# Optimization experiments

Measured on AMD Instinct MI355X. Metric: run time of the kernel, lower is better.

## Reference

```python
import jax, jax.numpy as jnp
import numpy as np

B, N, S, K, D = 8, 8192, 1024, 32, 64
RADIUS = 0.2
MLP = [64, 64, 128]
C_IN = 3 + D


def _fps(pts):
    # pts: [N,3] -> [S] farthest-point indices (deterministic start at index 0,
    # matching pytorch3d.sample_farthest_points default random_start_point=False)
    def body(carry, _):
        d, last = carry
        dd = jnp.sum((pts - pts[last]) ** 2, axis=-1)
        d = jnp.minimum(d, dd)
        return (d, jnp.argmax(d)), last
    init = (jnp.full((pts.shape[0],), 1e10, pts.dtype), jnp.asarray(0))
    _, idxs = jax.lax.scan(body, init, None, length=S)
    return idxs


def _ball_query(new_xyz, xyz):
    # new_xyz [B,S,3], xyz [B,N,3] -> idx [B,S,K]
    # classic PointNet++ ball query: first K points (by index order) within radius;
    # queries with fewer than K neighbors are padded by replicating the first hit.
    sqr = jnp.sum((new_xyz[:, :, None, :] - xyz[:, None, :, :]) ** 2, axis=-1)  # [B,S,N]
    cand = jnp.where(sqr <= RADIUS ** 2,
                     jnp.arange(N, dtype=jnp.int32)[None, None, :],
                     jnp.int32(N))
    idx = -jax.lax.top_k(-cand, K)[0]  # K smallest valid indices, ascending
    first = idx[..., :1]
    return jnp.where(idx == N, first, idx)


def _gather(arr, idx):
    # arr [B,N,C], idx [B,S,K] -> [B,S,K,C]
    return jax.vmap(lambda a, i: a[i])(arr, idx)


def _forward(xyz, points, attention, w0, b0, w1, b1, w2, b2):
    x = xyz.transpose(0, 2, 1)        # [B,N,3]
    p = points.transpose(0, 2, 1)     # [B,N,D]
    a = attention.transpose(0, 2, 1)  # [B,N,1]
    fps_idx = jax.vmap(_fps)(x)                      # [B,S]
    new_xyz = jax.vmap(lambda q, i: q[i])(x, fps_idx)  # [B,S,3]
    idx = _ball_query(new_xyz, x)                    # [B,S,K]
    g_norm = _gather(x, idx) - new_xyz[:, :, None, :]   # [B,S,K,3]
    feat = jnp.concatenate([g_norm, _gather(p, idx)], axis=-1)  # [B,S,K,3+D]
    new_att = jnp.mean(_gather(a, idx), axis=-2).reshape(x.shape[0], 1, -1)  # [B,1,S]
    # shared MLP (1x1 Conv2d == per-point dense), no BN (bn=False)
    h = jax.nn.relu(jnp.einsum('bskc,oc->bsko', feat, w0) + b0)
    h = jax.nn.relu(jnp.einsum('bskc,oc->bsko', h, w1) + b1)
    h = jax.nn.relu(jnp.einsum('bskc,oc->bsko', h, w2) + b2)
    new_points = jnp.max(h, axis=2)  # max-pool over nsample -> [B,S,C_out]
    return new_xyz.transpose(0, 2, 1), new_points.transpose(0, 2, 1), new_att


def setup_inputs() -> dict:
    key = jax.random.key(0)
    ks = jax.random.split(key, 9)
    xyz = jax.random.uniform(ks[0], (B, 3, N), dtype=jnp.float32)  # unit cube
    points = jax.random.normal(ks[1], (B, D, N), dtype=jnp.float32)
    attention = jax.random.uniform(ks[2], (B, 1, N), dtype=jnp.float32)
    cin = C_IN
    w0 = jax.random.normal(ks[3], (MLP[0], cin), dtype=jnp.float32) / np.sqrt(cin)
    b0 = jnp.zeros((MLP[0],), jnp.float32)
    w1 = jax.random.normal(ks[4], (MLP[1], MLP[0]), dtype=jnp.float32) / np.sqrt(MLP[0])
    b1 = jnp.zeros((MLP[1],), jnp.float32)
    w2 = jax.random.normal(ks[5], (MLP[2], MLP[1]), dtype=jnp.float32) / np.sqrt(MLP[1])
    b2 = jnp.zeros((MLP[2],), jnp.float32)
    return {"xyz": xyz, "points": points, "attention": attention,
            "w0": w0, "b0": b0, "w1": w1, "b1": b1, "w2": w2, "b2": b2}


def reference(xyz, points, attention, w0, b0, w1, b1, w2, b2):
    return _forward(xyz, points, attention, w0, b0, w1, b1, w2, b2)
```

## Files before the change

kernel.cpp:

```cpp
#include <hip/hip_runtime.h>

#define NPTS 8192
#define NSAMP 1024
#define NBATCH 8
#define KNB 32

typedef float f32x2 __attribute__((ext_vector_type(2)));
typedef unsigned long long u64;

__device__ __forceinline__ f32x2 pk_add(f32x2 a, f32x2 b) {
  f32x2 d; asm("v_pk_add_f32 %0, %1, %2" : "=v"(d) : "v"(a), "v"(b)); return d;
}
__device__ __forceinline__ f32x2 pk_mul(f32x2 a, f32x2 b) {
  f32x2 d; asm("v_pk_mul_f32 %0, %1, %2" : "=v"(d) : "v"(a), "v"(b)); return d;
}

#define DPP_FMAX_ROUND(v, CTRL)                                                        \
  do {                                                                                 \
    int _b = __float_as_int(v);                                                        \
    int _p = __builtin_amdgcn_update_dpp(_b, _b, CTRL, 0xF, 0xF, false);               \
    (v) = fmaxf((v), __int_as_float(_p));                                              \
  } while (0)

#define DPP_FMIN_ROUND(v, CTRL)                                                        \
  do {                                                                                 \
    int _b = __float_as_int(v);                                                        \
    int _p = __builtin_amdgcn_update_dpp(_b, _b, CTRL, 0xF, 0xF, false);               \
    (v) = fminf((v), __int_as_float(_p));                                              \
  } while (0)

#define DPP_UMIN_ROUND(v, CTRL)                                                        \
  do {                                                                                 \
    unsigned _p = (unsigned)__builtin_amdgcn_update_dpp((int)(v), (int)(v), CTRL,      \
                                                        0xF, 0xF, false);              \
    if (_p < (v)) (v) = _p;                                                            \
  } while (0)

#define DPP_MIN_ROUND(k, CTRL)                                                         \
  do {                                                                                 \
    unsigned _lo = (unsigned)(k), _hi = (unsigned)((k) >> 32);                         \
    unsigned _plo = (unsigned)__builtin_amdgcn_update_dpp((int)_lo, (int)_lo, CTRL,    \
                                                          0xF, 0xF, false);            \
    unsigned _phi = (unsigned)__builtin_amdgcn_update_dpp((int)_hi, (int)_hi, CTRL,    \
                                                          0xF, 0xF, false);            \
    u64 _ok = (((u64)_phi) << 32) | _plo;                                              \
    if (_ok < (k)) (k) = _ok;                                                          \
  } while (0)

__device__ __forceinline__ float sqdist_rn(float px, float py, float pz,
                                           float qx, float qy, float qz) {
  float dx = px - qx, dy = py - qy, dz = pz - qz;
  return __fadd_rn(__fadd_rn(__fmul_rn(dx, dx), __fmul_rn(dy, dy)), __fmul_rn(dz, dz));
}

__global__ __launch_bounds__(512) void fps_kernel(const float* __restrict__ xyz,
                                                  float* __restrict__ out_newxyz) {
  __shared__ __align__(16) char smem_raw[NPTS * 3 * 4];
  u64* sbuf = reinterpret_cast<u64*>(smem_raw);
  float* cds = reinterpret_cast<float*>(smem_raw);
  __shared__ u64 wkeys[2][8];

  const int b = blockIdx.x;
  const int tid = threadIdx.x;
  const int lane = tid & 63;
  const int wv = tid >> 6;
  const float* xb = xyz + (size_t)b * 3 * NPTS;

  for (int j = 0; j < 16; j++) {
    int n = tid + j * 512;
    float x = xb[n];
    sbuf[n] = (((u64)__float_as_uint(x)) << 32) | (u64)n;
  }
  __syncthreads();

  for (unsigned k = 2; k <= (unsigned)NPTS; k <<= 1) {
    for (unsigned jm = k >> 1; jm > 0; jm >>= 1) {
      for (int p = 0; p < 16; p++) {
        unsigned i = (unsigned)tid + (unsigned)p * 512u;
        unsigned ixj = i ^ jm;
        if (ixj > i) {
          u64 a = sbuf[i], c = sbuf[ixj];
          bool up = ((i & k) == 0);
          if ((a > c) == up) { sbuf[i] = c; sbuf[ixj] = a; }
        }
      }
      __syncthreads();
    }
  }

  f32x2 X2[8], Y2[8], Z2[8], D2[8];
  unsigned idxp[8];
  float txmin = 1e30f, txmax = -1e30f;
#pragma unroll
  for (int j = 0; j < 8; j++) {
    u64 k0 = sbuf[tid * 16 + 2 * j];
    u64 k1 = sbuf[tid * 16 + 2 * j + 1];
    unsigned n0 = (unsigned)k0 & 8191u, n1 = (unsigned)k1 & 8191u;
    float x0 = __uint_as_float((unsigned)(k0 >> 32));
    float x1 = __uint_as_float((unsigned)(k1 >> 32));
    X2[j].x = x0; X2[j].y = x1;
    Y2[j].x = xb[NPTS + n0];     Y2[j].y = xb[NPTS + n1];
    Z2[j].x = xb[2 * NPTS + n0]; Z2[j].y = xb[2 * NPTS + n1];
    D2[j].x = 1e10f;             D2[j].y = 1e10f;
    idxp[j] = n0 | (n1 << 16);
    txmin = fminf(txmin, fminf(x0, x1));
    txmax = fmaxf(txmax, fmaxf(x0, x1));
  }
  DPP_FMIN_ROUND(txmin, 0x111); DPP_FMIN_ROUND(txmin, 0x112);
  DPP_FMIN_ROUND(txmin, 0x114); DPP_FMIN_ROUND(txmin, 0x118);
  DPP_FMIN_ROUND(txmin, 0x142); DPP_FMIN_ROUND(txmin, 0x143);
  DPP_FMAX_ROUND(txmax, 0x111); DPP_FMAX_ROUND(txmax, 0x112);
  DPP_FMAX_ROUND(txmax, 0x114); DPP_FMAX_ROUND(txmax, 0x118);
  DPP_FMAX_ROUND(txmax, 0x142); DPP_FMAX_ROUND(txmax, 0x143);
  const float xlo = __int_as_float(__builtin_amdgcn_readlane(__float_as_int(txmin), 63));
  const float xhi = __int_as_float(__builtin_amdgcn_readlane(__float_as_int(txmax), 63));
  __syncthreads();

#pragma unroll
  for (int j = 0; j < 8; j++) {
    unsigned n0 = idxp[j] & 0xFFFFu, n1 = idxp[j] >> 16;
    cds[n0 * 3 + 0] = X2[j].x; cds[n0 * 3 + 1] = Y2[j].x; cds[n0 * 3 + 2] = Z2[j].x;
    cds[n1 * 3 + 0] = X2[j].y; cds[n1 * 3 + 1] = Y2[j].y; cds[n1 * 3 + 2] = Z2[j].y;
  }
  __syncthreads();

  float sx = cds[0], sy = cds[1], sz = cds[2];
  unsigned c0i = 0, c1i = 0;
  float bv_cache = 1e10f;
  u64 key_cache = ~0ull;

  for (int t = 0; t < NSAMP; t++) {
    float gap = fmaxf(fmaxf(xlo - sx, sx - xhi), 0.0f);
    float lb = __fmul_rn(gap, gap);

    if (lb < bv_cache) {
      f32x2 nqx, nqy, nqz;
      nqx.x = -sx; nqx.y = -sx;
      nqy.x = -sy; nqy.y = -sy;
      nqz.x = -sz; nqz.y = -sz;
      float bvx = -1.0f, bvy = -1.0f;
#pragma unroll
      for (int j = 0; j < 8; j++) {
        f32x2 dx = pk_add(X2[j], nqx);
        f32x2 dy = pk_add(Y2[j], nqy);
        f32x2 dz = pk_add(Z2[j], nqz);
        f32x2 dd = pk_add(pk_add(pk_mul(dx, dx), pk_mul(dy, dy)), pk_mul(dz, dz));
        float m0 = fminf(D2[j].x, dd.x);
        float m1 = fminf(D2[j].y, dd.y);
        D2[j].x = m0;
        D2[j].y = m1;
        bvx = fmaxf(bvx, m0);
        bvy = fmaxf(bvy, m1);
      }
      float bv = fmaxf(bvx, bvy);

      DPP_FMAX_ROUND(bv, 0x111);
      DPP_FMAX_ROUND(bv, 0x112);
      DPP_FMAX_ROUND(bv, 0x114);
      DPP_FMAX_ROUND(bv, 0x118);
      DPP_FMAX_ROUND(bv, 0x142);
      DPP_FMAX_ROUND(bv, 0x143);
      float wval = __int_as_float(__builtin_amdgcn_readlane(__float_as_int(bv), 63));

      unsigned cand = 0xFFFFFFFFu;
#pragma unroll
      for (int j = 0; j < 8; j++) {
        unsigned n0 = idxp[j] & 0xFFFFu, n1 = idxp[j] >> 16;
        if (D2[j].x == wval && n0 < cand) cand = n0;
        if (D2[j].y == wval && n1 < cand) cand = n1;
      }
      DPP_UMIN_ROUND(cand, 0x111);
      DPP_UMIN_ROUND(cand, 0x112);
      DPP_UMIN_ROUND(cand, 0x114);
      DPP_UMIN_ROUND(cand, 0x118);
      DPP_UMIN_ROUND(cand, 0x142);
      DPP_UMIN_ROUND(cand, 0x143);

      key_cache = (((u64)(~__float_as_uint(wval))) << 32) | (u64)cand;
      bv_cache = wval;
    }

    const int par = t & 1;
    if (lane == 63) wkeys[par][wv] = key_cache;
    __syncthreads();
    u64 k8 = wkeys[par][lane & 7];
    DPP_MIN_ROUND(k8, 0xB1);
    DPP_MIN_ROUND(k8, 0x4E);
    DPP_MIN_ROUND(k8, 0x141);
    unsigned wid = (unsigned)__builtin_amdgcn_readfirstlane((int)(unsigned)k8);

    if (t + 1 == tid) c0i = wid;
    if (t + 1 == tid + 512) c1i = wid;

    sx = cds[wid * 3 + 0];
    sy = cds[wid * 3 + 1];
    sz = cds[wid * 3 + 2];
  }

  {
    float ax = cds[c0i * 3 + 0], ay = cds[c0i * 3 + 1], az = cds[c0i * 3 + 2];
    float bx = cds[c1i * 3 + 0], by = cds[c1i * 3 + 1], bz = cds[c1i * 3 + 2];
    out_newxyz[(b * 3 + 0) * NSAMP + tid] = ax;
    out_newxyz[(b * 3 + 1) * NSAMP + tid] = ay;
    out_newxyz[(b * 3 + 2) * NSAMP + tid] = az;
    out_newxyz[(b * 3 + 0) * NSAMP + 512 + tid] = bx;
    out_newxyz[(b * 3 + 1) * NSAMP + 512 + tid] = by;
    out_newxyz[(b * 3 + 2) * NSAMP + 512 + tid] = bz;
  }
}

__global__ __launch_bounds__(256) void ballq_kernel(const float* __restrict__ xyz,
                                                    const float* __restrict__ att,
                                                    const float* __restrict__ newxyz,
                                                    int* __restrict__ idx_out,
                                                    float* __restrict__ att_out) {
  __shared__ int rowbuf[4][KNB];
  const int wv = threadIdx.x >> 6;
  const int lane = threadIdx.x & 63;
  const int g = blockIdx.x * 4 + wv;
  const int b = g >> 10;
  const int s = g & 1023;
  const float* xb = xyz + (size_t)b * 3 * NPTS;

  float qx = newxyz[(b * 3 + 0) * NSAMP + s];
  float qy = newxyz[(b * 3 + 1) * NSAMP + s];
  float qz = newxyz[(b * 3 + 2) * NSAMP + s];

  int have = 0;
  int firstn = 0;
  for (int c = 0; c < NPTS / 64; c++) {
    int n = c * 64 + lane;
    float dd = sqdist_rn(xb[n], xb[NPTS + n], xb[2 * NPTS + n], qx, qy, qz);
    bool inb = (dd <= 0.04f);
    unsigned long long m = __ballot(inb);
    if (have == 0 && m != 0ull) firstn = c * 64 + __builtin_ctzll(m);
    int pre = __popcll(m & ((1ull << lane) - 1ull));
    if (inb && (have + pre) < KNB) rowbuf[wv][have + pre] = n;
    have += __popcll(m);
    if (have >= KNB) break;
  }
  if (have > KNB) have = KNB;
  if (lane < KNB && lane >= have) rowbuf[wv][lane] = firstn;

  float av = 0.0f;
  if (lane < KNB) {
    int myidx = rowbuf[wv][lane];
    idx_out[(size_t)g * KNB + lane] = myidx;
    av = att[(size_t)b * NPTS + myidx];
  }
#pragma unroll
  for (int m = 1; m < 64; m <<= 1) av += __shfl_xor(av, m, 64);
  if (lane == 0) att_out[g] = av * 0.03125f;
}

__global__ __launch_bounds__(256) void mlp_kernel(
    const float* __restrict__ xyz, const float* __restrict__ pts,
    const float* __restrict__ newxyz, const int* __restrict__ idx,
    const float* __restrict__ w0, const float* __restrict__ b0,
    const float* __restrict__ w1, const float* __restrict__ b1,
    const float* __restrict__ w2, const float* __restrict__ b2,
    float* __restrict__ out_np) {
  const int g = blockIdx.x;
  const int b = g >> 10;
  const int s = g & 1023;
  const int t = threadIdx.x;

  __shared__ __align__(16) float feat[67 * 32];
  __shared__ __align__(16) float h0s[64 * 36];
  __shared__ __align__(16) float h1s[64 * 36];
  __shared__ int sidx[KNB];

  if (t < KNB) sidx[t] = idx[(size_t)g * KNB + t];
  __syncthreads();

  {
    int k = t & 31, rg = t >> 5;
    int n = sidx[k];
    const float* pb = pts + (size_t)b * 64 * NPTS;
    for (int r = rg; r < 67; r += 8) {
      float v;
      if (r < 3)
        v = xyz[((size_t)b * 3 + r) * NPTS + n] - newxyz[(b * 3 + r) * NSAMP + s];
      else
        v = pb[(size_t)(r - 3) * NPTS + n];
      feat[r * 32 + k] = v;
    }
  }
  __syncthreads();

  const int kq = t & 7;
  const int og = t >> 3;

  {
    float a0[8];
    float bu = b0[2 * og], bw = b0[2 * og + 1];
    a0[0] = a0[1] = a0[2] = a0[3] = bu;
    a0[4] = a0[5] = a0[6] = a0[7] = bw;
    const float* wr0 = w0 + (2 * og) * 67;
    const float* wr1 = wr0 + 67;
    for (int c = 0; c < 67; c++) {
      float4 f = *(const float4*)&feat[c * 32 + kq * 4];
      float u = wr0[c], v = wr1[c];
      a0[0] = fmaf(u, f.x, a0[0]); a0[1] = fmaf(u, f.y, a0[1]);
      a0[2] = fmaf(u, f.z, a0[2]); a0[3] = fmaf(u, f.w, a0[3]);
      a0[4] = fmaf(v, f.x, a0[4]); a0[5] = fmaf(v, f.y, a0[5]);
      a0[6] = fmaf(v, f.z, a0[6]); a0[7] = fmaf(v, f.w, a0[7]);
    }
    float4 r0, r1;
    r0.x = fmaxf(a0[0], 0.f); r0.y = fmaxf(a0[1], 0.f);
    r0.z = fmaxf(a0[2], 0.f); r0.w = fmaxf(a0[3], 0.f);
    r1.x = fmaxf(a0[4], 0.f); r1.y = fmaxf(a0[5], 0.f);
    r1.z = fmaxf(a0[6], 0.f); r1.w = fmaxf(a0[7], 0.f);
    *(float4*)&h0s[(2 * og) * 36 + kq * 4] = r0;
    *(float4*)&h0s[(2 * og + 1) * 36 + kq * 4] = r1;
  }
  __syncthreads();

  {
    float a1[8];
    float bu = b1[2 * og], bw = b1[2 * og + 1];
    a1[0] = a1[1] = a1[2] = a1[3] = bu;
    a1[4] = a1[5] = a1[6] = a1[7] = bw;
    const float* wr0 = w1 + (2 * og) * 64;
    const float* wr1 = wr0 + 64;
    for (int c = 0; c < 64; c++) {
      float4 f = *(const float4*)&h0s[c * 36 + kq * 4];
      float u = wr0[c], v = wr1[c];
      a1[0] = fmaf(u, f.x, a1[0]); a1[1] = fmaf(u, f.y, a1[1]);
      a1[2] = fmaf(u, f.z, a1[2]); a1[3] = fmaf(u, f.w, a1[3]);
      a1[4] = fmaf(v, f.x, a1[4]); a1[5] = fmaf(v, f.y, a1[5]);
      a1[6] = fmaf(v, f.z, a1[6]); a1[7] = fmaf(v, f.w, a1[7]);
    }
    float4 r0, r1;
    r0.x = fmaxf(a1[0], 0.f); r0.y = fmaxf(a1[1], 0.f);
    r0.z = fmaxf(a1[2], 0.f); r0.w = fmaxf(a1[3], 0.f);
    r1.x = fmaxf(a1[4], 0.f); r1.y = fmaxf(a1[5], 0.f);
    r1.z = fmaxf(a1[6], 0.f); r1.w = fmaxf(a1[7], 0.f);
    *(float4*)&h1s[(2 * og) * 36 + kq * 4] = r0;
    *(float4*)&h1s[(2 * og + 1) * 36 + kq * 4] = r1;
  }
  __syncthreads();

  {
    const int kq2 = t & 3;
    const int og2 = t >> 2;
    float a2[16];
    float bu = b2[2 * og2], bw = b2[2 * og2 + 1];
#pragma unroll
    for (int i = 0; i < 8; i++) { a2[i] = bu; a2[8 + i] = bw; }
    const float* wr0 = w2 + (2 * og2) * 64;
    const float* wr1 = wr0 + 64;
    for (int c = 0; c < 64; c++) {
      float4 fA = *(const float4*)&h1s[c * 36 + kq2 * 8];
      float4 fB = *(const float4*)&h1s[c * 36 + kq2 * 8 + 4];
      float u = wr0[c], v = wr1[c];
      a2[0] = fmaf(u, fA.x, a2[0]);  a2[1] = fmaf(u, fA.y, a2[1]);
      a2[2] = fmaf(u, fA.z, a2[2]);  a2[3] = fmaf(u, fA.w, a2[3]);
      a2[4] = fmaf(u, fB.x, a2[4]);  a2[5] = fmaf(u, fB.y, a2[5]);
      a2[6] = fmaf(u, fB.z, a2[6]);  a2[7] = fmaf(u, fB.w, a2[7]);
      a2[8] = fmaf(v, fA.x, a2[8]);  a2[9] = fmaf(v, fA.y, a2[9]);
      a2[10] = fmaf(v, fA.z, a2[10]); a2[11] = fmaf(v, fA.w, a2[11]);
      a2[12] = fmaf(v, fB.x, a2[12]); a2[13] = fmaf(v, fB.y, a2[13]);
      a2[14] = fmaf(v, fB.z, a2[14]); a2[15] = fmaf(v, fB.w, a2[15]);
    }
    float m0 = a2[0], m1 = a2[8];
#pragma unroll
    for (int i = 1; i < 8; i++) { m0 = fmaxf(m0, a2[i]); m1 = fmaxf(m1, a2[8 + i]); }
    m0 = fmaxf(m0, 0.f);
    m1 = fmaxf(m1, 0.f);
    m0 = fmaxf(m0, __shfl_xor(m0, 1, 64));
    m0 = fmaxf(m0, __shfl_xor(m0, 2, 64));
    m1 = fmaxf(m1, __shfl_xor(m1, 1, 64));
    m1 = fmaxf(m1, __shfl_xor(m1, 2, 64));
    if (kq2 == 0) {
      out_np[((size_t)b * 128 + 2 * og2) * NSAMP + s] = m0;
      out_np[((size_t)b * 128 + 2 * og2 + 1) * NSAMP + s] = m1;
    }
  }
}

extern "C" void kernel_launch(void* const* d_in, const int* in_sizes, int n_in,
                              void* d_out, int out_size, void* d_ws, size_t ws_size,
                              hipStream_t stream) {
  (void)in_sizes; (void)n_in; (void)out_size; (void)ws_size;
  const float* xyz = (const float*)d_in[0];
  const float* pts = (const float*)d_in[1];
  const float* att = (const float*)d_in[2];
  const float* w0 = (const float*)d_in[3];
  const float* b0 = (const float*)d_in[4];
  const float* w1 = (const float*)d_in[5];
  const float* b1 = (const float*)d_in[6];
  const float* w2 = (const float*)d_in[7];
  const float* b2 = (const float*)d_in[8];

  float* out = (float*)d_out;
  float* out_newxyz = out;
  float* out_newpts = out + NBATCH * 3 * NSAMP;
  float* out_att = out + NBATCH * 3 * NSAMP + NBATCH * 128 * NSAMP;
  int* idx_ws = (int*)d_ws;

  fps_kernel<<<NBATCH, 512, 0, stream>>>(xyz, out_newxyz);
  ballq_kernel<<<(NBATCH * NSAMP) / 4, 256, 0, stream>>>(xyz, att, out_newxyz, idx_ws, out_att);
  mlp_kernel<<<NBATCH * NSAMP, 256, 0, stream>>>(xyz, pts, out_newxyz, idx_ws,
                                                 w0, b0, w1, b1, w2, b2, out_newpts);
}
```

Measured before the change: 1.160 ms.

## Fuse FPS, ball query and MLP into persistent producer-consumer kernel

Merges the three kernels into one persistent launch. 8 blocks run farthest-point sampling and publish progress per batch through atomics in global memory. 120 consumer blocks poll that progress and run ball query plus the MLP on pairs of samples as soon as they are available. This overlaps the serial FPS stage with downstream work and removes the index workspace round trip. The cost is fewer consumer blocks, spin-wait overhead, and a deadlock risk if producer and consumer blocks are not co-resident.

```diff
diff --git a/kernel.cpp b/kernel.cpp
--- a/kernel.cpp
+++ b/kernel.cpp
@@ -4,6 +4,8 @@
 #define NSAMP 1024
 #define NBATCH 8
 #define KNB 32
+#define NPROD 8
+#define NCONS 120
 
 typedef float f32x2 __attribute__((ext_vector_type(2)));
 typedef unsigned long long u64;
@@ -53,328 +55,324 @@
   return __fadd_rn(__fadd_rn(__fmul_rn(dx, dx), __fmul_rn(dy, dy)), __fmul_rn(dz, dz));
 }
 
-__global__ __launch_bounds__(512) void fps_kernel(const float* __restrict__ xyz,
-                                                  float* __restrict__ out_newxyz) {
-  __shared__ __align__(16) char smem_raw[NPTS * 3 * 4];
-  u64* sbuf = reinterpret_cast<u64*>(smem_raw);
-  float* cds = reinterpret_cast<float*>(smem_raw);
-  __shared__ u64 wkeys[2][8];
-
-  const int b = blockIdx.x;
-  const int tid = threadIdx.x;
-  const int lane = tid & 63;
-  const int wv = tid >> 6;
-  const float* xb = xyz + (size_t)b * 3 * NPTS;
-
-  for (int j = 0; j < 16; j++) {
-    int n = tid + j * 512;
-    float x = xb[n];
-    sbuf[n] = (((u64)__float_as_uint(x)) << 32) | (u64)n;
-  }
-  __syncthreads();
-
-  for (unsigned k = 2; k <= (unsigned)NPTS; k <<= 1) {
-    for (unsigned jm = k >> 1; jm > 0; jm >>= 1) {
-      for (int p = 0; p < 16; p++) {
-        unsigned i = (unsigned)tid + (unsigned)p * 512u;
-        unsigned ixj = i ^ jm;
-        if (ixj > i) {
-          u64 a = sbuf[i], c = sbuf[ixj];
-          bool up = ((i & k) == 0);
-          if ((a > c) == up) { sbuf[i] = c; sbuf[ixj] = a; }
-        }
-      }
-      __syncthreads();
-    }
-  }
-
-  f32x2 X2[8], Y2[8], Z2[8], D2[8];
-  unsigned idxp[8];
-  float txmin = 1e30f, txmax = -1e30f;
-#pragma unroll
-  for (int j = 0; j < 8; j++) {
-    u64 k0 = sbuf[tid * 16 + 2 * j];
-    u64 k1 = sbuf[tid * 16 + 2 * j + 1];
-    unsigned n0 = (unsigned)k0 & 8191u, n1 = (unsigned)k1 & 8191u;
-    float x0 = __uint_as_float((unsigned)(k0 >> 32));
-    float x1 = __uint_as_float((unsigned)(k1 >> 32));
-    X2[j].x = x0; X2[j].y = x1;
-    Y2[j].x = xb[NPTS + n0];     Y2[j].y = xb[NPTS + n1];
-    Z2[j].x = xb[2 * NPTS + n0]; Z2[j].y = xb[2 * NPTS + n1];
-    D2[j].x = 1e10f;             D2[j].y = 1e10f;
-    idxp[j] = n0 | (n1 << 16);
-    txmin = fminf(txmin, fminf(x0, x1));
-    txmax = fmaxf(txmax, fmaxf(x0, x1));
-  }
-  DPP_FMIN_ROUND(txmin, 0x111); DPP_FMIN_ROUND(txmin, 0x112);
-  DPP_FMIN_ROUND(txmin, 0x114); DPP_FMIN_ROUND(txmin, 0x118);
-  DPP_FMIN_ROUND(txmin, 0x142); DPP_FMIN_ROUND(txmin, 0x143);
-  DPP_FMAX_ROUND(txmax, 0x111); DPP_FMAX_ROUND(txmax, 0x112);
-  DPP_FMAX_ROUND(txmax, 0x114); DPP_FMAX_ROUND(txmax, 0x118);
-  DPP_FMAX_ROUND(txmax, 0x142); DPP_FMAX_ROUND(txmax, 0x143);
-  const float xlo = __int_as_float(__builtin_amdgcn_readlane(__float_as_int(txmin), 63));
-  const float xhi = __int_as_float(__builtin_amdgcn_readlane(__float_as_int(txmax), 63));
-  __syncthreads();
-
-#pragma unroll
-  for (int j = 0; j < 8; j++) {
-    unsigned n0 = idxp[j] & 0xFFFFu, n1 = idxp[j] >> 16;
-    cds[n0 * 3 + 0] = X2[j].x; cds[n0 * 3 + 1] = Y2[j].x; cds[n0 * 3 + 2] = Z2[j].x;
-    cds[n1 * 3 + 0] = X2[j].y; cds[n1 * 3 + 1] = Y2[j].y; cds[n1 * 3 + 2] = Z2[j].y;
-  }
-  __syncthreads();
-
-  float sx = cds[0], sy = cds[1], sz = cds[2];
-  unsigned c0i = 0, c1i = 0;
-  float bv_cache = 1e10f;
-  u64 key_cache = ~0ull;
-
-  for (int t = 0; t < NSAMP; t++) {
-    float gap = fmaxf(fmaxf(xlo - sx, sx - xhi), 0.0f);
-    float lb = __fmul_rn(gap, gap);
-
-    if (lb < bv_cache) {
-      f32x2 nqx, nqy, nqz;
-      nqx.x = -sx; nqx.y = -sx;
-      nqy.x = -sy; nqy.y = -sy;
-      nqz.x = -sz; nqz.y = -sz;
-      float bvx = -1.0f, bvy = -1.0f;
-#pragma unroll
-      for (int j = 0; j < 8; j++) {
-        f32x2 dx = pk_add(X2[j], nqx);
-        f32x2 dy = pk_add(Y2[j], nqy);
-        f32x2 dz = pk_add(Z2[j], nqz);
-        f32x2 dd = pk_add(pk_add(pk_mul(dx, dx), pk_mul(dy, dy)), pk_mul(dz, dz));
-        float m0 = fminf(D2[j].x, dd.x);
-        float m1 = fminf(D2[j].y, dd.y);
-        D2[j].x = m0;
-        D2[j].y = m1;
-        bvx = fmaxf(bvx, m0);
-        bvy = fmaxf(bvy, m1);
-      }
-      float bv = fmaxf(bvx, bvy);
-
-      DPP_FMAX_ROUND(bv, 0x111);
-      DPP_FMAX_ROUND(bv, 0x112);
-      DPP_FMAX_ROUND(bv, 0x114);
-      DPP_FMAX_ROUND(bv, 0x118);
-      DPP_FMAX_ROUND(bv, 0x142);
-      DPP_FMAX_ROUND(bv, 0x143);
-      float wval = __int_as_float(__builtin_amdgcn_readlane(__float_as_int(bv), 63));
-
-      unsigned cand = 0xFFFFFFFFu;
-#pragma unroll
-      for (int j = 0; j < 8; j++) {
-        unsigned n0 = idxp[j] & 0xFFFFu, n1 = idxp[j] >> 16;
-        if (D2[j].x == wval && n0 < cand) cand = n0;
-        if (D2[j].y == wval && n1 < cand) cand = n1;
-      }
-      DPP_UMIN_ROUND(cand, 0x111);
-      DPP_UMIN_ROUND(cand, 0x112);
-      DPP_UMIN_ROUND(cand, 0x114);
-      DPP_UMIN_ROUND(cand, 0x118);
-      DPP_UMIN_ROUND(cand, 0x142);
-      DPP_UMIN_ROUND(cand, 0x143);
-
-      key_cache = (((u64)(~__float_as_uint(wval))) << 32) | (u64)cand;
-      bv_cache = wval;
-    }
-
-    const int par = t & 1;
-    if (lane == 63) wkeys[par][wv] = key_cache;
-    __syncthreads();
-    u64 k8 = wkeys[par][lane & 7];
-    DPP_MIN_ROUND(k8, 0xB1);
-    DPP_MIN_ROUND(k8, 0x4E);
-    DPP_MIN_ROUND(k8, 0x141);
-    unsigned wid = (unsigned)__builtin_amdgcn_readfirstlane((int)(unsigned)k8);
-
-    if (t + 1 == tid) c0i = wid;
-    if (t + 1 == tid + 512) c1i = wid;
-
-    sx = cds[wid * 3 + 0];
-    sy = cds[wid * 3 + 1];
-    sz = cds[wid * 3 + 2];
-  }
-
-  {
-    float ax = cds[c0i * 3 + 0], ay = cds[c0i * 3 + 1], az = cds[c0i * 3 + 2];
-    float bx = cds[c1i * 3 + 0], by = cds[c1i * 3 + 1], bz = cds[c1i * 3 + 2];
-    out_newxyz[(b * 3 + 0) * NSAMP + tid] = ax;
-    out_newxyz[(b * 3 + 1) * NSAMP + tid] = ay;
-    out_newxyz[(b * 3 + 2) * NSAMP + tid] = az;
-    out_newxyz[(b * 3 + 0) * NSAMP + 512 + tid] = bx;
-    out_newxyz[(b * 3 + 1) * NSAMP + 512 + tid] = by;
-    out_newxyz[(b * 3 + 2) * NSAMP + 512 + tid] = bz;
-  }
-}
-
-__global__ __launch_bounds__(256) void ballq_kernel(const float* __restrict__ xyz,
-                                                    const float* __restrict__ att,
-                                                    const float* __restrict__ newxyz,
-                                                    int* __restrict__ idx_out,
-                                                    float* __restrict__ att_out) {
-  __shared__ int rowbuf[4][KNB];
-  const int wv = threadIdx.x >> 6;
-  const int lane = threadIdx.x & 63;
-  const int g = blockIdx.x * 4 + wv;
-  const int b = g >> 10;
-  const int s = g & 1023;
-  const float* xb = xyz + (size_t)b * 3 * NPTS;
-
-  float qx = newxyz[(b * 3 + 0) * NSAMP + s];
-  float qy = newxyz[(b * 3 + 1) * NSAMP + s];
-  float qz = newxyz[(b * 3 + 2) * NSAMP + s];
-
-  int have = 0;
-  int firstn = 0;
-  for (int c = 0; c < NPTS / 64; c++) {
-    int n = c * 64 + lane;
-    float dd = sqdist_rn(xb[n], xb[NPTS + n], xb[2 * NPTS + n], qx, qy, qz);
-    bool inb = (dd <= 0.04f);
-    unsigned long long m = __ballot(inb);
-    if (have == 0 && m != 0ull) firstn = c * 64 + __builtin_ctzll(m);
-    int pre = __popcll(m & ((1ull << lane) - 1ull));
-    if (inb && (have + pre) < KNB) rowbuf[wv][have + pre] = n;
-    have += __popcll(m);
-    if (have >= KNB) break;
-  }
-  if (have > KNB) have = KNB;
-  if (lane < KNB && lane >= have) rowbuf[wv][lane] = firstn;
-
-  float av = 0.0f;
-  if (lane < KNB) {
-    int myidx = rowbuf[wv][lane];
-    idx_out[(size_t)g * KNB + lane] = myidx;
-    av = att[(size_t)b * NPTS + myidx];
-  }
-#pragma unroll
-  for (int m = 1; m < 64; m <<= 1) av += __shfl_xor(av, m, 64);
-  if (lane == 0) att_out[g] = av * 0.03125f;
-}
-
-__global__ __launch_bounds__(256) void mlp_kernel(
+__global__ __launch_bounds__(512, 1) void fused_kernel(
     const float* __restrict__ xyz, const float* __restrict__ pts,
-    const float* __restrict__ newxyz, const int* __restrict__ idx,
+    const float* __restrict__ att,
     const float* __restrict__ w0, const float* __restrict__ b0,
     const float* __restrict__ w1, const float* __restrict__ b1,
     const float* __restrict__ w2, const float* __restrict__ b2,
-    float* __restrict__ out_np) {
-  const int g = blockIdx.x;
-  const int b = g >> 10;
-  const int s = g & 1023;
-  const int t = threadIdx.x;
-
-  __shared__ __align__(16) float feat[67 * 32];
-  __shared__ __align__(16) float h0s[64 * 36];
-  __shared__ __align__(16) float h1s[64 * 36];
-  __shared__ int sidx[KNB];
-
-  if (t < KNB) sidx[t] = idx[(size_t)g * KNB + t];
-  __syncthreads();
-
-  {
-    int k = t & 31, rg = t >> 5;
-    int n = sidx[k];
-    const float* pb = pts + (size_t)b * 64 * NPTS;
-    for (int r = rg; r < 67; r += 8) {
-      float v;
-      if (r < 3)
-        v = xyz[((size_t)b * 3 + r) * NPTS + n] - newxyz[(b * 3 + r) * NSAMP + s];
-      else
-        v = pb[(size_t)(r - 3) * NPTS + n];
-      feat[r * 32 + k] = v;
-    }
-  }
-  __syncthreads();
-
-  const int kq = t & 7;
-  const int og = t >> 3;
-
-  {
-    float a0[8];
-    float bu = b0[2 * og], bw = b0[2 * og + 1];
-    a0[0] = a0[1] = a0[2] = a0[3] = bu;
-    a0[4] = a0[5] = a0[6] = a0[7] = bw;
-    const float* wr0 = w0 + (2 * og) * 67;
-    const float* wr1 = wr0 + 67;
-    for (int c = 0; c < 67; c++) {
-      float4 f = *(const float4*)&feat[c * 32 + kq * 4];
-      float u = wr0[c], v = wr1[c];
-      a0[0] = fmaf(u, f.x, a0[0]); a0[1] = fmaf(u, f.y, a0[1]);
-      a0[2] = fmaf(u, f.z, a0[2]); a0[3] = fmaf(u, f.w, a0[3]);
-      a0[4] = fmaf(v, f.x, a0[4]); a0[5] = fmaf(v, f.y, a0[5]);
-      a0[6] = fmaf(v, f.z, a0[6]); a0[7] = fmaf(v, f.w, a0[7]);
-    }
-    float4 r0, r1;
-    r0.x = fmaxf(a0[0], 0.f); r0.y = fmaxf(a0[1], 0.f);
-    r0.z = fmaxf(a0[2], 0.f); r0.w = fmaxf(a0[3], 0.f);
-    r1.x = fmaxf(a0[4], 0.f); r1.y = fmaxf(a0[5], 0.f);
-    r1.z = fmaxf(a0[6], 0.f); r1.w = fmaxf(a0[7], 0.f);
-    *(float4*)&h0s[(2 * og) * 36 + kq * 4] = r0;
-    *(float4*)&h0s[(2 * og + 1) * 36 + kq * 4] = r1;
-  }
-  __syncthreads();
-
-  {
-    float a1[8];
-    float bu = b1[2 * og], bw = b1[2 * og + 1];
-    a1[0] = a1[1] = a1[2] = a1[3] = bu;
-    a1[4] = a1[5] = a1[6] = a1[7] = bw;
-    const float* wr0 = w1 + (2 * og) * 64;
-    const float* wr1 = wr0 + 64;
-    for (int c = 0; c < 64; c++) {
-      float4 f = *(const float4*)&h0s[c * 36 + kq * 4];
-      float u = wr0[c], v = wr1[c];
-      a1[0] = fmaf(u, f.x, a1[0]); a1[1] = fmaf(u, f.y, a1[1]);
-      a1[2] = fmaf(u, f.z, a1[2]); a1[3] = fmaf(u, f.w, a1[3]);
-      a1[4] = fmaf(v, f.x, a1[4]); a1[5] = fmaf(v, f.y, a1[5]);
-      a1[6] = fmaf(v, f.z, a1[6]); a1[7] = fmaf(v, f.w, a1[7]);
-    }
-    float4 r0, r1;
-    r0.x = fmaxf(a1[0], 0.f); r0.y = fmaxf(a1[1], 0.f);
-    r0.z = fmaxf(a1[2], 0.f); r0.w = fmaxf(a1[3], 0.f);
-    r1.x = fmaxf(a1[4], 0.f); r1.y = fmaxf(a1[5], 0.f);
-    r1.z = fmaxf(a1[6], 0.f); r1.w = fmaxf(a1[7], 0.f);
-    *(float4*)&h1s[(2 * og) * 36 + kq * 4] = r0;
-    *(float4*)&h1s[(2 * og + 1) * 36 + kq * 4] = r1;
-  }
-  __syncthreads();
-
-  {
-    const int kq2 = t & 3;
-    const int og2 = t >> 2;
-    float a2[16];
-    float bu = b2[2 * og2], bw = b2[2 * og2 + 1];
-#pragma unroll
-    for (int i = 0; i < 8; i++) { a2[i] = bu; a2[8 + i] = bw; }
-    const float* wr0 = w2 + (2 * og2) * 64;
-    const float* wr1 = wr0 + 64;
-    for (int c = 0; c < 64; c++) {
-      float4 fA = *(const float4*)&h1s[c * 36 + kq2 * 8];
-      float4 fB = *(const float4*)&h1s[c * 36 + kq2 * 8 + 4];
-      float u = wr0[c], v = wr1[c];
-      a2[0] = fmaf(u, fA.x, a2[0]);  a2[1] = fmaf(u, fA.y, a2[1]);
-      a2[2] = fmaf(u, fA.z, a2[2]);  a2[3] = fmaf(u, fA.w, a2[3]);
-      a2[4] = fmaf(u, fB.x, a2[4]);  a2[5] = fmaf(u, fB.y, a2[5]);
-      a2[6] = fmaf(u, fB.z, a2[6]);  a2[7] = fmaf(u, fB.w, a2[7]);
-      a2[8] = fmaf(v, fA.x, a2[8]);  a2[9] = fmaf(v, fA.y, a2[9]);
-      a2[10] = fmaf(v, fA.z, a2[10]); a2[11] = fmaf(v, fA.w, a2[11]);
-      a2[12] = fmaf(v, fB.x, a2[12]); a2[13] = fmaf(v, fB.y, a2[13]);
-      a2[14] = fmaf(v, fB.z, a2[14]); a2[15] = fmaf(v, fB.w, a2[15]);
-    }
-    float m0 = a2[0], m1 = a2[8];
-#pragma unroll
-    for (int i = 1; i < 8; i++) { m0 = fmaxf(m0, a2[i]); m1 = fmaxf(m1, a2[8 + i]); }
-    m0 = fmaxf(m0, 0.f);
-    m1 = fmaxf(m1, 0.f);
-    m0 = fmaxf(m0, __shfl_xor(m0, 1, 64));
-    m0 = fmaxf(m0, __shfl_xor(m0, 2, 64));
-    m1 = fmaxf(m1, __shfl_xor(m1, 1, 64));
-    m1 = fmaxf(m1, __shfl_xor(m1, 2, 64));
-    if (kq2 == 0) {
-      out_np[((size_t)b * 128 + 2 * og2) * NSAMP + s] = m0;
-      out_np[((size_t)b * 128 + 2 * og2 + 1) * NSAMP + s] = m1;
+    float* __restrict__ out_newxyz, float* __restrict__ out_np,
+    float* __restrict__ att_out, unsigned* __restrict__ prog) {
+  __shared__ __align__(16) char smem_raw[98304];
+  __shared__ u64 wkeys[2][8];
+  __shared__ int sidxs[2][KNB];
+
+  const int tid = threadIdx.x;
+
+  if (blockIdx.x < NPROD) {
+    u64* sbuf = reinterpret_cast<u64*>(smem_raw);
+    float* cds = reinterpret_cast<float*>(smem_raw);
+
+    const int b = blockIdx.x;
+    const int lane = tid & 63;
+    const int wv = tid >> 6;
+    const float* xb = xyz + (size_t)b * 3 * NPTS;
+
+    for (int j = 0; j < 16; j++) {
+      int n = tid + j * 512;
+      float x = xb[n];
+      sbuf[n] = (((u64)__float_as_uint(x)) << 32) | (u64)n;
+    }
+    __syncthreads();
+
+    for (unsigned k = 2; k <= (unsigned)NPTS; k <<= 1) {
+      for (unsigned jm = k >> 1; jm > 0; jm >>= 1) {
+        for (int p = 0; p < 16; p++) {
+          unsigned i = (unsigned)tid + (unsigned)p * 512u;
+          unsigned ixj = i ^ jm;
+          if (ixj > i) {
+            u64 a = sbuf[i], c = sbuf[ixj];
+            bool up = ((i & k) == 0);
+            if ((a > c) == up) { sbuf[i] = c; sbuf[ixj] = a; }
+          }
+        }
+        __syncthreads();
+      }
+    }
+
+    f32x2 X2[8], Y2[8], Z2[8], D2[8];
+    unsigned idxp[8];
+    float txmin = 1e30f, txmax = -1e30f;
+#pragma unroll
+    for (int j = 0; j < 8; j++) {
+      u64 k0 = sbuf[tid * 16 + 2 * j];
+      u64 k1 = sbuf[tid * 16 + 2 * j + 1];
+      unsigned n0 = (unsigned)k0 & 8191u, n1 = (unsigned)k1 & 8191u;
+      float x0 = __uint_as_float((unsigned)(k0 >> 32));
+      float x1 = __uint_as_float((unsigned)(k1 >> 32));
+      X2[j].x = x0; X2[j].y = x1;
+      Y2[j].x = xb[NPTS + n0];     Y2[j].y = xb[NPTS + n1];
+      Z2[j].x = xb[2 * NPTS + n0]; Z2[j].y = xb[2 * NPTS + n1];
+      D2[j].x = 1e10f;             D2[j].y = 1e10f;
+      idxp[j] = n0 | (n1 << 16);
+      txmin = fminf(txmin, fminf(x0, x1));
+      txmax = fmaxf(txmax, fmaxf(x0, x1));
+    }
+    DPP_FMIN_ROUND(txmin, 0x111); DPP_FMIN_ROUND(txmin, 0x112);
+    DPP_FMIN_ROUND(txmin, 0x114); DPP_FMIN_ROUND(txmin, 0x118);
+    DPP_FMIN_ROUND(txmin, 0x142); DPP_FMIN_ROUND(txmin, 0x143);
+    DPP_FMAX_ROUND(txmax, 0x111); DPP_FMAX_ROUND(txmax, 0x112);
+    DPP_FMAX_ROUND(txmax, 0x114); DPP_FMAX_ROUND(txmax, 0x118);
+    DPP_FMAX_ROUND(txmax, 0x142); DPP_FMAX_ROUND(txmax, 0x143);
+    const float xlo = __int_as_float(__builtin_amdgcn_readlane(__float_as_int(txmin), 63));
+    const float xhi = __int_as_float(__builtin_amdgcn_readlane(__float_as_int(txmax), 63));
+    __syncthreads();
+
+#pragma unroll
+    for (int j = 0; j < 8; j++) {
+      unsigned n0 = idxp[j] & 0xFFFFu, n1 = idxp[j] >> 16;
+      cds[n0 * 3 + 0] = X2[j].x; cds[n0 * 3 + 1] = Y2[j].x; cds[n0 * 3 + 2] = Z2[j].x;
+      cds[n1 * 3 + 0] = X2[j].y; cds[n1 * 3 + 1] = Y2[j].y; cds[n1 * 3 + 2] = Z2[j].y;
+    }
+    __syncthreads();
+
+    float sx = cds[0], sy = cds[1], sz = cds[2];
+    float bv_cache = 1e10f;
+    u64 key_cache = ~0ull;
+
+    for (int t = 0; t < NSAMP; t++) {
+      if (tid == 0) {
+        out_newxyz[(b * 3 + 0) * NSAMP + t] = sx;
+        out_newxyz[(b * 3 + 1) * NSAMP + t] = sy;
+        out_newxyz[(b * 3 + 2) * NSAMP + t] = sz;
+      }
+
+      float gap = fmaxf(fmaxf(xlo - sx, sx - xhi), 0.0f);
+      float lb = __fmul_rn(gap, gap);
+
+      if (lb < bv_cache) {
+        f32x2 nqx, nqy, nqz;
+        nqx.x = -sx; nqx.y = -sx;
+        nqy.x = -sy; nqy.y = -sy;
+        nqz.x = -sz; nqz.y = -sz;
+        float bvx = -1.0f, bvy = -1.0f;
+#pragma unroll
+        for (int j = 0; j < 8; j++) {
+          f32x2 dx = pk_add(X2[j], nqx);
+          f32x2 dy = pk_add(Y2[j], nqy);
+          f32x2 dz = pk_add(Z2[j], nqz);
+          f32x2 dd = pk_add(pk_add(pk_mul(dx, dx), pk_mul(dy, dy)), pk_mul(dz, dz));
+          float m0 = fminf(D2[j].x, dd.x);
+          float m1 = fminf(D2[j].y, dd.y);
+          D2[j].x = m0;
+          D2[j].y = m1;
+          bvx = fmaxf(bvx, m0);
+          bvy = fmaxf(bvy, m1);
+        }
+        float bv = fmaxf(bvx, bvy);
+
+        DPP_FMAX_ROUND(bv, 0x111);
+        DPP_FMAX_ROUND(bv, 0x112);
+        DPP_FMAX_ROUND(bv, 0x114);
+        DPP_FMAX_ROUND(bv, 0x118);
+        DPP_FMAX_ROUND(bv, 0x142);
+        DPP_FMAX_ROUND(bv, 0x143);
+        float wval = __int_as_float(__builtin_amdgcn_readlane(__float_as_int(bv), 63));
+
+        unsigned cand = 0xFFFFFFFFu;
+#pragma unroll
+        for (int j = 0; j < 8; j++) {
+          unsigned n0 = idxp[j] & 0xFFFFu, n1 = idxp[j] >> 16;
+          if (D2[j].y == wval && n1 < cand) cand = n1;
+          if (D2[j].x == wval && n0 < cand) cand = n0;
+        }
+        DPP_UMIN_ROUND(cand, 0x111);
+        DPP_UMIN_ROUND(cand, 0x112);
+        DPP_UMIN_ROUND(cand, 0x114);
+        DPP_UMIN_ROUND(cand, 0x118);
+        DPP_UMIN_ROUND(cand, 0x142);
+        DPP_UMIN_ROUND(cand, 0x143);
+
+        key_cache = (((u64)(~__float_as_uint(wval))) << 32) | (u64)cand;
+        bv_cache = wval;
+        if (lane == 63) wkeys[t & 1][wv] = key_cache;
+      } else {
+        if (lane == 63) wkeys[t & 1][wv] = key_cache;
+      }
+      __syncthreads();
+      u64 k8 = wkeys[t & 1][lane & 7];
+      DPP_MIN_ROUND(k8, 0xB1);
+      DPP_MIN_ROUND(k8, 0x4E);
+      DPP_MIN_ROUND(k8, 0x141);
+      unsigned wid = (unsigned)__builtin_amdgcn_readfirstlane((int)(unsigned)k8);
+
+      sx = cds[wid * 3 + 0];
+      sy = cds[wid * 3 + 1];
+      sz = cds[wid * 3 + 2];
+
+      if ((t & 7) == 7 && tid == 0) {
+        __threadfence();
+        atomicExch(&prog[b], (unsigned)(t + 1));
+      }
+    }
+  } else {
+    float* smemF = reinterpret_cast<float*>(smem_raw);
+    const int tm = tid >> 8;
+    const int t = tid & 255;
+    float* feat = smemF + tm * 6784;
+    float* h0s = feat + 2144;
+    float* h1s = h0s + 2304;
+
+    for (int p = (int)blockIdx.x - NPROD; p < (NBATCH * NSAMP) / 2; p += NCONS) {
+      const int gA = 2 * p;
+      const int b = gA >> 10;
+      const int sA = gA & 1023;
+      if (tid == 0) {
+        unsigned need = (unsigned)(sA + 2);
+        while (atomicAdd(&prog[b], 0u) < need) __builtin_amdgcn_s_sleep(64);
+        __threadfence();
+      }
+      __syncthreads();
+
+      const int g = gA + tm;
+      const int s = sA + tm;
+      const float* xb = xyz + (size_t)b * 3 * NPTS;
+
+      if (t < 64) {
+        const int lane = t;
+        float qx = out_newxyz[(b * 3 + 0) * NSAMP + s];
+        float qy = out_newxyz[(b * 3 + 1) * NSAMP + s];
+        float qz = out_newxyz[(b * 3 + 2) * NSAMP + s];
+        int have = 0;
+        int firstn = 0;
+        for (int c = 0; c < NPTS / 64; c++) {
+          int n = c * 64 + lane;
+          float dd = sqdist_rn(xb[n], xb[NPTS + n], xb[2 * NPTS + n], qx, qy, qz);
+          bool inb = (dd <= 0.04f);
+          unsigned long long m = __ballot(inb);
+          if (have == 0 && m != 0ull) firstn = c * 64 + __builtin_ctzll(m);
+          int pre = __popcll(m & ((1ull << lane) - 1ull));
+          if (inb && (have + pre) < KNB) sidxs[tm][have + pre] = n;
+          have += __popcll(m);
+          if (have >= KNB) break;
+        }
+        if (have > KNB) have = KNB;
+        if (lane < KNB && lane >= have) sidxs[tm][lane] = firstn;
+
+        float av = 0.0f;
+        if (lane < KNB) av = att[(size_t)b * NPTS + sidxs[tm][lane]];
+#pragma unroll
+        for (int m = 1; m < 64; m <<= 1) av += __shfl_xor(av, m, 64);
+        if (lane == 0) att_out[g] = av * 0.03125f;
+      }
+      __syncthreads();
+
+      {
+        int k = t & 31, rg = t >> 5;
+        int n = sidxs[tm][k];
+        const float* pb = pts + (size_t)b * 64 * NPTS;
+        for (int r = rg; r < 67; r += 8) {
+          float v;
+          if (r < 3)
+            v = xyz[((size_t)b * 3 + r) * NPTS + n] -
+                out_newxyz[(b * 3 + r) * NSAMP + s];
+          else
+            v = pb[(size_t)(r - 3) * NPTS + n];
+          feat[r * 32 + k] = v;
+        }
+      }
+      __syncthreads();
+
+      const int kq = t & 7;
+      const int og = t >> 3;
+
+      {
+        float a0[8];
+        float bu = b0[2 * og], bw = b0[2 * og + 1];
+        a0[0] = a0[1] = a0[2] = a0[3] = bu;
+        a0[4] = a0[5] = a0[6] = a0[7] = bw;
+        const float* wr0 = w0 + (2 * og) * 67;
+        const float* wr1 = wr0 + 67;
+        for (int c = 0; c < 67; c++) {
+          float4 f = *(const float4*)&feat[c * 32 + kq * 4];
+          float u = wr0[c], v = wr1[c];
+          a0[0] = fmaf(u, f.x, a0[0]); a0[1] = fmaf(u, f.y, a0[1]);
+          a0[2] = fmaf(u, f.z, a0[2]); a0[3] = fmaf(u, f.w, a0[3]);
+          a0[4] = fmaf(v, f.x, a0[4]); a0[5] = fmaf(v, f.y, a0[5]);
+          a0[6] = fmaf(v, f.z, a0[6]); a0[7] = fmaf(v, f.w, a0[7]);
+        }
+        float4 r0, r1;
+        r0.x = fmaxf(a0[0], 0.f); r0.y = fmaxf(a0[1], 0.f);
+        r0.z = fmaxf(a0[2], 0.f); r0.w = fmaxf(a0[3], 0.f);
+        r1.x = fmaxf(a0[4], 0.f); r1.y = fmaxf(a0[5], 0.f);
+        r1.z = fmaxf(a0[6], 0.f); r1.w = fmaxf(a0[7], 0.f);
+        *(float4*)&h0s[(2 * og) * 36 + kq * 4] = r0;
+        *(float4*)&h0s[(2 * og + 1) * 36 + kq * 4] = r1;
+      }
+      __syncthreads();
+
+      {
+        float a1[8];
+        float bu = b1[2 * og], bw = b1[2 * og + 1];
+        a1[0] = a1[1] = a1[2] = a1[3] = bu;
+        a1[4] = a1[5] = a1[6] = a1[7] = bw;
+        const float* wr0 = w1 + (2 * og) * 64;
+        const float* wr1 = wr0 + 64;
+        for (int c = 0; c < 64; c++) {
+          float4 f = *(const float4*)&h0s[c * 36 + kq * 4];
+          float u = wr0[c], v = wr1[c];
+          a1[0] = fmaf(u, f.x, a1[0]); a1[1] = fmaf(u, f.y, a1[1]);
+          a1[2] = fmaf(u, f.z, a1[2]); a1[3] = fmaf(u, f.w, a1[3]);
+          a1[4] = fmaf(v, f.x, a1[4]); a1[5] = fmaf(v, f.y, a1[5]);
+          a1[6] = fmaf(v, f.z, a1[6]); a1[7] = fmaf(v, f.w, a1[7]);
+        }
+        float4 r0, r1;
+        r0.x = fmaxf(a1[0], 0.f); r0.y = fmaxf(a1[1], 0.f);
+        r0.z = fmaxf(a1[2], 0.f); r0.w = fmaxf(a1[3], 0.f);
+        r1.x = fmaxf(a1[4], 0.f); r1.y = fmaxf(a1[5], 0.f);
+        r1.z = fmaxf(a1[6], 0.f); r1.w = fmaxf(a1[7], 0.f);
+        *(float4*)&h1s[(2 * og) * 36 + kq * 4] = r0;
+        *(float4*)&h1s[(2 * og + 1) * 36 + kq * 4] = r1;
+      }
+      __syncthreads();
+
+      {
+        const int kq2 = t & 3;
+        const int og2 = t >> 2;
+        float a2[16];
+        float bu = b2[2 * og2], bw = b2[2 * og2 + 1];
+#pragma unroll
+        for (int i = 0; i < 8; i++) { a2[i] = bu; a2[8 + i] = bw; }
+        const float* wr0 = w2 + (2 * og2) * 64;
+        const float* wr1 = wr0 + 64;
+        for (int c = 0; c < 64; c++) {
+          float4 fA = *(const float4*)&h1s[c * 36 + kq2 * 8];
+          float4 fB = *(const float4*)&h1s[c * 36 + kq2 * 8 + 4];
+          float u = wr0[c], v = wr1[c];
+          a2[0] = fmaf(u, fA.x, a2[0]);  a2[1] = fmaf(u, fA.y, a2[1]);
+          a2[2] = fmaf(u, fA.z, a2[2]);  a2[3] = fmaf(u, fA.w, a2[3]);
+          a2[4] = fmaf(u, fB.x, a2[4]);  a2[5] = fmaf(u, fB.y, a2[5]);
+          a2[6] = fmaf(u, fB.z, a2[6]);  a2[7] = fmaf(u, fB.w, a2[7]);
+          a2[8] = fmaf(v, fA.x, a2[8]);  a2[9] = fmaf(v, fA.y, a2[9]);
+          a2[10] = fmaf(v, fA.z, a2[10]); a2[11] = fmaf(v, fA.w, a2[11]);
+          a2[12] = fmaf(v, fB.x, a2[12]); a2[13] = fmaf(v, fB.y, a2[13]);
+          a2[14] = fmaf(v, fB.z, a2[14]); a2[15] = fmaf(v, fB.w, a2[15]);
+        }
+        float m0 = a2[0], m1 = a2[8];
+#pragma unroll
+        for (int i = 1; i < 8; i++) { m0 = fmaxf(m0, a2[i]); m1 = fmaxf(m1, a2[8 + i]); }
+        m0 = fmaxf(m0, 0.f);
+        m1 = fmaxf(m1, 0.f);
+        m0 = fmaxf(m0, __shfl_xor(m0, 1, 64));
+        m0 = fmaxf(m0, __shfl_xor(m0, 2, 64));
+        m1 = fmaxf(m1, __shfl_xor(m1, 1, 64));
+        m1 = fmaxf(m1, __shfl_xor(m1, 2, 64));
+        if (kq2 == 0) {
+          out_np[((size_t)b * 128 + 2 * og2) * NSAMP + s] = m0;
+          out_np[((size_t)b * 128 + 2 * og2 + 1) * NSAMP + s] = m1;
+        }
+      }
+      __syncthreads();
     }
   }
 }
@@ -397,10 +395,10 @@
   float* out_newxyz = out;
   float* out_newpts = out + NBATCH * 3 * NSAMP;
   float* out_att = out + NBATCH * 3 * NSAMP + NBATCH * 128 * NSAMP;
-  int* idx_ws = (int*)d_ws;
-
-  fps_kernel<<<NBATCH, 512, 0, stream>>>(xyz, out_newxyz);
-  ballq_kernel<<<(NBATCH * NSAMP) / 4, 256, 0, stream>>>(xyz, att, out_newxyz, idx_ws, out_att);
-  mlp_kernel<<<NBATCH * NSAMP, 256, 0, stream>>>(xyz, pts, out_newxyz, idx_ws,
-                                                 w0, b0, w1, b1, w2, b2, out_newpts);
+  unsigned* prog = (unsigned*)d_ws;
+
+  hipMemsetAsync(prog, 0, NBATCH * sizeof(unsigned), stream);
+  fused_kernel<<<NPROD + NCONS, 512, 0, stream>>>(
+      xyz, pts, att, w0, b0, w1, b1, w2, b2,
+      out_newxyz, out_newpts, out_att, prog);
 }
```

Measured after the change: 2.969 ms. 2.56x slower.
